# Optimization experiments

Measured on AMD Instinct MI355X. Metric: run time of the kernel, lower is better.

The kernel has to match this reference:

```python
import jax, jax.numpy as jnp
import numpy as np

EPS = 1e-18

_SOBEL_H = jnp.array([[-1., -2., -1.], [0., 0., 0.], [1., 2., 1.]], dtype=jnp.float32)


def _sobel_mag(x, eps):
    # x: [B,1,H,W]; depth-1 3x3 conv with 'same' padding, two fixed kernels
    wh = _SOBEL_H.reshape(1, 1, 3, 3).astype(x.dtype)   # horizontal kernel
    wv = _SOBEL_H.T.reshape(1, 1, 3, 3).astype(x.dtype)  # vertical kernel
    dn = jax.lax.conv_dimension_numbers(x.shape, wh.shape, ('NCHW', 'OIHW', 'NCHW'))
    gv = jax.lax.conv_general_dilated(x, wv, (1, 1), 'SAME', dimension_numbers=dn)
    gh = jax.lax.conv_general_dilated(x, wh, (1, 1), 'SAME', dimension_numbers=dn)
    return jnp.sqrt(gv * gv + gh * gh + eps)


def setup_inputs() -> dict:
    key = jax.random.key(0)
    k1, k2 = jax.random.split(key)
    shape = (64, 1, 512, 512)
    y_p = jax.random.uniform(k1, shape, dtype=jnp.float32)
    y_t = jax.random.uniform(k2, shape, dtype=jnp.float32)
    return {"y_p": y_p, "y_t": y_t}


def reference(y_p, y_t):
    eps = EPS
    ypg = _sobel_mag(y_p, eps)
    ytg = _sobel_mag(y_t, eps)
    out = (ytg - ypg) ** 2
    mask = (out == 0.0).astype(out.dtype)
    out = out + mask * eps
    out = jnp.sqrt(out + eps) * (1.0 - mask)
    return jnp.mean(out)
```

## Files before the change

kernel.cpp:

```cpp
#include <hip/hip_runtime.h>

#define IMG_W 512
#define IMG_H 512
#define BATCH 64
#define ROWS_PER_WAVE 8
#define SLABS (IMG_H / ROWS_PER_WAVE)
#define NBLOCKS (BATCH * SLABS)
#define NPIX (BATCH * IMG_W * IMG_H)

__device__ __forceinline__ float fast_sqrtf(float x) {
    return __builtin_amdgcn_sqrtf(x);
}

__global__ __launch_bounds__(64) void sobel_loss_kernel(
    const float* __restrict__ yp, const float* __restrict__ yt,
    float* __restrict__ bsums)
{
    const int lane = threadIdx.x;
    const int bid  = blockIdx.x;
    const int b    = bid >> 6;
    const int slab = bid & (SLABS - 1);
    const int y0   = slab * ROWS_PER_WAVE;
    const int x0   = lane << 3;

    const float* __restrict__ imgp = yp + (size_t)b * (IMG_W * IMG_H);
    const float* __restrict__ imgt = yt + (size_t)b * (IMG_W * IMG_H);

    float hp[3][10], ht[3][10];
    float4 A0p, B0p, A0t, B0t;
    float4 A1p, B1p, A1t, B1t;

#define ISSUE(S, Y)                                                            \
    do {                                                                       \
        int yy = (Y);                                                          \
        if (yy >= 0 && yy < IMG_H) {                                           \
            const float* rp = imgp + (size_t)yy * IMG_W + x0;                  \
            const float* rt = imgt + (size_t)yy * IMG_W + x0;                  \
            A##S##p = *(const float4*)rp;                                      \
            B##S##p = *(const float4*)(rp + 4);                                \
            A##S##t = *(const float4*)rt;                                      \
            B##S##t = *(const float4*)(rt + 4);                                \
        } else {                                                               \
            A##S##p = {0.f, 0.f, 0.f, 0.f}; B##S##p = {0.f, 0.f, 0.f, 0.f};   \
            A##S##t = {0.f, 0.f, 0.f, 0.f}; B##S##t = {0.f, 0.f, 0.f, 0.f};   \
        }                                                                      \
    } while (0)

#define ASSEMBLE(S, R)                                                         \
    do {                                                                       \
        float lp  = __shfl_up(B##S##p.w, 1, 64);                               \
        float rp_ = __shfl_down(A##S##p.x, 1, 64);                             \
        float lt  = __shfl_up(B##S##t.w, 1, 64);                               \
        float rt_ = __shfl_down(A##S##t.x, 1, 64);                             \
        if (lane == 0)  { lp = 0.f; lt = 0.f; }                                \
        if (lane == 63) { rp_ = 0.f; rt_ = 0.f; }                              \
        hp[R][0] = lp;      ht[R][0] = lt;                                     \
        hp[R][1] = A##S##p.x; hp[R][2] = A##S##p.y;                            \
        hp[R][3] = A##S##p.z; hp[R][4] = A##S##p.w;                            \
        hp[R][5] = B##S##p.x; hp[R][6] = B##S##p.y;                            \
        hp[R][7] = B##S##p.z; hp[R][8] = B##S##p.w;                            \
        ht[R][1] = A##S##t.x; ht[R][2] = A##S##t.y;                            \
        ht[R][3] = A##S##t.z; ht[R][4] = A##S##t.w;                            \
        ht[R][5] = B##S##t.x; ht[R][6] = B##S##t.y;                            \
        ht[R][7] = B##S##t.z; ht[R][8] = B##S##t.w;                            \
        hp[R][9] = rp_;     ht[R][9] = rt_;                                    \
    } while (0)

    float lsum = 0.f;

#define COMPUTE(S0, S1, S2)                                                    \
    do {                                                                       \
        float cp[10], ct[10];                                                  \
        _Pragma("unroll")                                                      \
        for (int k = 0; k < 10; ++k) {                                         \
            cp[k] = fmaf(2.f, hp[S1][k], hp[S0][k]) + hp[S2][k];               \
            ct[k] = fmaf(2.f, ht[S1][k], ht[S0][k]) + ht[S2][k];               \
        }                                                                      \
        _Pragma("unroll")                                                      \
        for (int j = 0; j < 8; ++j) {                                          \
            float tp  = fmaf(2.f, hp[S2][j + 1], hp[S2][j]) + hp[S2][j + 2];   \
            float bp_ = fmaf(2.f, hp[S0][j + 1], hp[S0][j]) + hp[S0][j + 2];   \
            float ghp = tp - bp_;                                              \
            float gvp = cp[j + 2] - cp[j];                                     \
            float magp = fast_sqrtf(fmaf(gvp, gvp, fmaf(ghp, ghp, 1e-18f)));   \
            float tt  = fmaf(2.f, ht[S2][j + 1], ht[S2][j]) + ht[S2][j + 2];   \
            float bt_ = fmaf(2.f, ht[S0][j + 1], ht[S0][j]) + ht[S0][j + 2];   \
            float ght = tt - bt_;                                              \
            float gvt = ct[j + 2] - ct[j];                                     \
            float magt = fast_sqrtf(fmaf(gvt, gvt, fmaf(ght, ght, 1e-18f)));   \
            lsum += fabsf(magt - magp);         \
        }                                                                      \
    } while (0)

    ISSUE(0, y0 - 1);
    ISSUE(1, y0);
    ASSEMBLE(0, 0);  ISSUE(0, y0 + 1);
    ASSEMBLE(1, 1);  ISSUE(1, y0 + 2);

    ASSEMBLE(0, 2);  ISSUE(0, y0 + 3);  COMPUTE(0, 1, 2);
    ASSEMBLE(1, 0);  ISSUE(1, y0 + 4);  COMPUTE(1, 2, 0);
    ASSEMBLE(0, 1);  ISSUE(0, y0 + 5);  COMPUTE(2, 0, 1);
    ASSEMBLE(1, 2);  ISSUE(1, y0 + 6);  COMPUTE(0, 1, 2);
    ASSEMBLE(0, 0);  ISSUE(0, y0 + 7);  COMPUTE(1, 2, 0);
    ASSEMBLE(1, 1);  ISSUE(1, y0 + 8);  COMPUTE(2, 0, 1);
    ASSEMBLE(0, 2);                     COMPUTE(0, 1, 2);
    ASSEMBLE(1, 0);                     COMPUTE(1, 2, 0);

#undef ISSUE
#undef ASSEMBLE
#undef COMPUTE

#pragma unroll
    for (int off = 32; off > 0; off >>= 1)
        lsum += __shfl_down(lsum, off, 64);
    if (lane == 0)
        bsums[bid] = lsum;
}

__global__ __launch_bounds__(256) void reduce_final(
    const float* __restrict__ bsums, float* __restrict__ out)
{
    __shared__ float wred[4];
    const int tid = threadIdx.x;
    float s = 0.f;
    for (int i = tid; i < NBLOCKS; i += 256) s += bsums[i];
#pragma unroll
    for (int off = 32; off > 0; off >>= 1)
        s += __shfl_down(s, off, 64);
    if ((tid & 63) == 0) wred[tid >> 6] = s;
    __syncthreads();
    if (tid == 0)
        out[0] = (wred[0] + wred[1] + wred[2] + wred[3]) * (1.0f / (float)NPIX);
}

extern "C" void kernel_launch(void* const* d_in, const int* in_sizes, int n_in,
                              void* d_out, int out_size, void* d_ws, size_t ws_size,
                              hipStream_t stream) {
    const float* yp = (const float*)d_in[0];
    const float* yt = (const float*)d_in[1];
    float* out = (float*)d_out;

    float* bsums = (float*)d_ws;
    sobel_loss_kernel<<<NBLOCKS, 64, 0, stream>>>(yp, yt, bsums);
    reduce_final<<<1, 256, 0, stream>>>(bsums, out);
}
```

Baseline: 150.1 us.

## Halve rows per wave and issue all row loads upfront

Each wave now processes 4 output rows instead of 8, doubling the block count, and the block-index decode changes to match. All five needed input rows (plus one reused slot) are loaded at the start so more memory requests are in flight. Row arrays are built directly from the loaded registers rather than copied into a rotating buffer. The cost is more halo re-reads (6 rows loaded per 4 output rows instead of 10 per 8) and more register pressure, in exchange for more memory-level parallelism and more waves.

Result: no change. 152.1 us (+1.4%).

```diff
diff --git a/kernel.cpp b/kernel.cpp
--- a/kernel.cpp
+++ b/kernel.cpp
@@ -3,7 +3,7 @@
 #define IMG_W 512
 #define IMG_H 512
 #define BATCH 64
-#define ROWS_PER_WAVE 8
+#define ROWS_PER_WAVE 4
 #define SLABS (IMG_H / ROWS_PER_WAVE)
 #define NBLOCKS (BATCH * SLABS)
 #define NPIX (BATCH * IMG_W * IMG_H)
@@ -18,7 +18,7 @@
 {
     const int lane = threadIdx.x;
     const int bid  = blockIdx.x;
-    const int b    = bid >> 6;
+    const int b    = bid >> 7;
     const int slab = bid & (SLABS - 1);
     const int y0   = slab * ROWS_PER_WAVE;
     const int x0   = lane << 3;
@@ -26,9 +26,10 @@
     const float* __restrict__ imgp = yp + (size_t)b * (IMG_W * IMG_H);
     const float* __restrict__ imgt = yt + (size_t)b * (IMG_W * IMG_H);
 
-    float hp[3][10], ht[3][10];
-    float4 A0p, B0p, A0t, B0t;
-    float4 A1p, B1p, A1t, B1t;
+    float4 A0p, B0p, A0t, B0t, A1p, B1p, A1t, B1t, A2p, B2p, A2t, B2t;
+    float4 A3p, B3p, A3t, B3t, A4p, B4p, A4t, B4t;
+    float  l0p, r0p, l0t, r0t, l1p, r1p, l1t, r1t, l2p, r2p, l2t, r2t;
+    float  l3p, r3p, l3t, r3t, l4p, r4p, l4t, r4t;
 
 #define ISSUE(S, Y)                                                            \
     do {                                                                       \
@@ -46,45 +47,42 @@
         }                                                                      \
     } while (0)
 
-#define ASSEMBLE(S, R)                                                         \
+#define HALO(S)                                                                \
     do {                                                                       \
-        float lp  = __shfl_up(B##S##p.w, 1, 64);                               \
-        float rp_ = __shfl_down(A##S##p.x, 1, 64);                             \
-        float lt  = __shfl_up(B##S##t.w, 1, 64);                               \
-        float rt_ = __shfl_down(A##S##t.x, 1, 64);                             \
-        if (lane == 0)  { lp = 0.f; lt = 0.f; }                                \
-        if (lane == 63) { rp_ = 0.f; rt_ = 0.f; }                              \
-        hp[R][0] = lp;      ht[R][0] = lt;                                     \
-        hp[R][1] = A##S##p.x; hp[R][2] = A##S##p.y;                            \
-        hp[R][3] = A##S##p.z; hp[R][4] = A##S##p.w;                            \
-        hp[R][5] = B##S##p.x; hp[R][6] = B##S##p.y;                            \
-        hp[R][7] = B##S##p.z; hp[R][8] = B##S##p.w;                            \
-        ht[R][1] = A##S##t.x; ht[R][2] = A##S##t.y;                            \
-        ht[R][3] = A##S##t.z; ht[R][4] = A##S##t.w;                            \
-        ht[R][5] = B##S##t.x; ht[R][6] = B##S##t.y;                            \
-        ht[R][7] = B##S##t.z; ht[R][8] = B##S##t.w;                            \
-        hp[R][9] = rp_;     ht[R][9] = rt_;                                    \
+        l##S##p = __shfl_up(B##S##p.w, 1, 64);                                 \
+        r##S##p = __shfl_down(A##S##p.x, 1, 64);                               \
+        l##S##t = __shfl_up(B##S##t.w, 1, 64);                                 \
+        r##S##t = __shfl_down(A##S##t.x, 1, 64);                               \
+        if (lane == 0)  { l##S##p = 0.f; l##S##t = 0.f; }                      \
+        if (lane == 63) { r##S##p = 0.f; r##S##t = 0.f; }                      \
     } while (0)
+
+#define ROW_ARR(NAME, R, IMG)                                                  \
+    const float NAME[10] = { l##R##IMG,                                        \
+        A##R##IMG.x, A##R##IMG.y, A##R##IMG.z, A##R##IMG.w,                    \
+        B##R##IMG.x, B##R##IMG.y, B##R##IMG.z, B##R##IMG.w, r##R##IMG };
 
     float lsum = 0.f;
 
-#define COMPUTE(S0, S1, S2)                                                    \
+#define COMPUTE(Ra, Rb, Rc)                                                    \
     do {                                                                       \
+        ROW_ARR(w0p, Ra, p) ROW_ARR(w1p, Rb, p) ROW_ARR(w2p, Rc, p)            \
+        ROW_ARR(w0t, Ra, t) ROW_ARR(w1t, Rb, t) ROW_ARR(w2t, Rc, t)            \
         float cp[10], ct[10];                                                  \
         _Pragma("unroll")                                                      \
         for (int k = 0; k < 10; ++k) {                                         \
-            cp[k] = fmaf(2.f, hp[S1][k], hp[S0][k]) + hp[S2][k];               \
-            ct[k] = fmaf(2.f, ht[S1][k], ht[S0][k]) + ht[S2][k];               \
+            cp[k] = fmaf(2.f, w1p[k], w0p[k]) + w2p[k];                        \
+            ct[k] = fmaf(2.f, w1t[k], w0t[k]) + w2t[k];                        \
         }                                                                      \
         _Pragma("unroll")                                                      \
         for (int j = 0; j < 8; ++j) {                                          \
-            float tp  = fmaf(2.f, hp[S2][j + 1], hp[S2][j]) + hp[S2][j + 2];   \
-            float bp_ = fmaf(2.f, hp[S0][j + 1], hp[S0][j]) + hp[S0][j + 2];   \
+            float tp  = fmaf(2.f, w2p[j + 1], w2p[j]) + w2p[j + 2];            \
+            float bp_ = fmaf(2.f, w0p[j + 1], w0p[j]) + w0p[j + 2];            \
             float ghp = tp - bp_;                                              \
             float gvp = cp[j + 2] - cp[j];                                     \
             float magp = fast_sqrtf(fmaf(gvp, gvp, fmaf(ghp, ghp, 1e-18f)));   \
-            float tt  = fmaf(2.f, ht[S2][j + 1], ht[S2][j]) + ht[S2][j + 2];   \
-            float bt_ = fmaf(2.f, ht[S0][j + 1], ht[S0][j]) + ht[S0][j + 2];   \
+            float tt  = fmaf(2.f, w2t[j + 1], w2t[j]) + w2t[j + 2];            \
+            float bt_ = fmaf(2.f, w0t[j + 1], w0t[j]) + w0t[j + 2];            \
             float ght = tt - bt_;                                              \
             float gvt = ct[j + 2] - ct[j];                                     \
             float magt = fast_sqrtf(fmaf(gvt, gvt, fmaf(ght, ght, 1e-18f)));   \
@@ -94,20 +92,20 @@
 
     ISSUE(0, y0 - 1);
     ISSUE(1, y0);
-    ASSEMBLE(0, 0);  ISSUE(0, y0 + 1);
-    ASSEMBLE(1, 1);  ISSUE(1, y0 + 2);
+    ISSUE(2, y0 + 1);
+    ISSUE(3, y0 + 2);
+    ISSUE(4, y0 + 3);
 
-    ASSEMBLE(0, 2);  ISSUE(0, y0 + 3);  COMPUTE(0, 1, 2);
-    ASSEMBLE(1, 0);  ISSUE(1, y0 + 4);  COMPUTE(1, 2, 0);
-    ASSEMBLE(0, 1);  ISSUE(0, y0 + 5);  COMPUTE(2, 0, 1);
-    ASSEMBLE(1, 2);  ISSUE(1, y0 + 6);  COMPUTE(0, 1, 2);
-    ASSEMBLE(0, 0);  ISSUE(0, y0 + 7);  COMPUTE(1, 2, 0);
-    ASSEMBLE(1, 1);  ISSUE(1, y0 + 8);  COMPUTE(2, 0, 1);
-    ASSEMBLE(0, 2);                     COMPUTE(0, 1, 2);
-    ASSEMBLE(1, 0);                     COMPUTE(1, 2, 0);
+    HALO(0); HALO(1); HALO(2);
+    COMPUTE(0, 1, 2);
+    ISSUE(0, y0 + 4);
+    HALO(3); COMPUTE(1, 2, 3);
+    HALO(4); COMPUTE(2, 3, 4);
+    HALO(0); COMPUTE(3, 4, 0);
 
 #undef ISSUE
-#undef ASSEMBLE
+#undef HALO
+#undef ROW_ARR
 #undef COMPUTE
 
 #pragma unroll
```
